# Kernel tuning notes

Measured on AMD Instinct MI355X. Metric: run time of the kernel, lower is better.

## Reference

```python
import jax, jax.numpy as jnp
import numpy as np

T = 4096          # tokens (batch*seq)
D = 768           # moe_intermediate_size (token hidden dim)
I = 2048          # intermediate_size (FFN inner dim)
E = 8             # num_experts


def setup_inputs() -> dict:
    key = jax.random.key(0)
    k_x, k_p, k_g, k_u, k_d = jax.random.split(key, 5)
    hidden_states = jax.random.normal(k_x, (T, D), dtype=jnp.float32)
    position_index = jax.random.randint(k_p, (T,), 0, E, dtype=jnp.int64)
    behavior_index = jnp.zeros((T,), dtype=jnp.int64)  # unused (behavior_injection=False)
    s = 0.02
    # torch Linear weight layout: [out_features, in_features]
    gate_w = jax.random.normal(k_g, (E, I, D), dtype=jnp.float32) * s
    up_w = jax.random.normal(k_u, (E, I, D), dtype=jnp.float32) * s
    down_w = jax.random.normal(k_d, (E, D, I), dtype=jnp.float32) * s
    return {
        "hidden_states": hidden_states,
        "position_index": position_index,
        "behavior_index": behavior_index,
        "gate_w": gate_w,
        "up_w": up_w,
        "down_w": down_w,
    }


def reference(hidden_states, position_index, behavior_index, gate_w, up_w, down_w):
    # Sparse MoE dispatch: each token routed to exactly one expert by position_index.
    # Dropout rate is 0.0 (eval) -> identity. behavior_injection=False -> behavior_index unused.
    num_experts = gate_w.shape[0]
    out = jnp.zeros_like(hidden_states)
    for e in range(num_experts):  # structural loop over fixed expert count
        mask = (position_index == e)[:, None]          # [T, 1]
        g = hidden_states @ gate_w[e].T                 # [T, I]
        u = hidden_states @ up_w[e].T                   # [T, I]
        y = (jax.nn.silu(g) * u) @ down_w[e].T          # [T, D]
        out = out + jnp.where(mask, y, 0.0)             # scatter-combine
    return out
```

## Files before the change

### kernel.cpp

```cpp
#include <hip/hip_runtime.h>
#include <hip/hip_bf16.h>

#define T_TOK 4096
#define DDIM  768
#define IDIM  2048
#define NEXP  8

typedef __attribute__((ext_vector_type(8))) short  bfrag;
typedef __attribute__((ext_vector_type(4))) float  ffrag;

static __device__ __forceinline__ unsigned short f2bf(float f) {
    union { float f; unsigned u; } v; v.f = f;
    unsigned r = v.u + 0x7FFFu + ((v.u >> 16) & 1u);
    return (unsigned short)(r >> 16);
}

static __device__ __forceinline__ unsigned cvt2(float x, float y) {
    return (unsigned)f2bf(x) | ((unsigned)f2bf(y) << 16);
}

__global__ void k_sort(const int* __restrict__ pos, int* __restrict__ ws_i,
                       int* __restrict__ perm) {
    __shared__ int hist[NEXP], cursor[NEXP];
    const int tid  = threadIdx.x;
    const int lane = tid & 63;
    if (tid < NEXP) hist[tid] = 0;
    __syncthreads();
    for (int i = tid; i < T_TOK; i += 1024) {
        int e = pos[i];
        #pragma unroll
        for (int ee = 0; ee < NEXP; ++ee) {
            unsigned long long m = __ballot(e == ee);
            if (e == ee && lane == (__ffsll((long long)m) - 1))
                atomicAdd(&hist[ee], __popcll(m));
        }
    }
    __syncthreads();
    if (tid == 0) {
        int s = 0;
        for (int e = 0; e < NEXP; ++e) {
            cursor[e] = s;
            ws_i[e] = hist[e];
            ws_i[16 + e] = s;
            s += hist[e];
        }
        ws_i[16 + NEXP] = s;
    }
    __syncthreads();
    for (int i = tid; i < T_TOK; i += 1024) {
        int e = pos[i];
        int p = 0;
        #pragma unroll
        for (int ee = 0; ee < NEXP; ++ee) {
            unsigned long long m = __ballot(e == ee);
            if (e == ee) {
                int leader = __ffsll((long long)m) - 1;
                int rank = __popcll(m & ((1ull << lane) - 1ull));
                int base = 0;
                if (lane == leader) base = atomicAdd(&cursor[ee], __popcll(m));
                base = __shfl(base, leader);
                p = base + rank;
            }
        }
        perm[p] = i;
    }
}

__global__ void k_gather(const float* __restrict__ x, const int* __restrict__ perm,
                         unsigned short* __restrict__ xg) {
    int p = blockIdx.x;
    int tok = perm[p];
    int j = threadIdx.x * 4;
    const float4 v = *reinterpret_cast<const float4*>(x + (size_t)tok * DDIM + j);
    uint2 o;
    o.x = cvt2(v.x, v.y);
    o.y = cvt2(v.z, v.w);
    *reinterpret_cast<uint2*>(xg + (size_t)p * DDIM + j) = o;
}

__launch_bounds__(256, 2)
__global__ void k_gemm1(const unsigned short* __restrict__ xg,
                        const float* __restrict__ gate_w,
                        const float* __restrict__ up_w,
                        unsigned short* __restrict__ hg,
                        const int* __restrict__ ws_i) {
    const int e   = blockIdx.z;
    const int cnt = ws_i[e];
    if (cnt == 0) return;
    const int nmt = (cnt + 127) >> 7;
    const int mg  = blockIdx.y;
    if (mg >= nmt) return;
    const int off = ws_i[16 + e];
    const int n0  = blockIdx.x * 64;

    const int tid  = threadIdx.x;
    const int lane = tid & 63;
    const int wave = tid >> 6;
    const int wm   = wave & 1;
    const int wn   = wave >> 1;

    __shared__ __align__(16) unsigned short lsA[128 * 56];
    __shared__ __align__(16) unsigned short lsG[64 * 56];
    __shared__ __align__(16) unsigned short lsU[64 * 56];

    const float* gate_e = gate_w + (size_t)e * (IDIM * DDIM);
    const float* up_e   = up_w   + (size_t)e * (IDIM * DDIM);

    const int ar = tid >> 2;
    const int aq = tid & 3;
    const int br = tid >> 3;
    const int bq = tid & 7;

    const float* gp0 = gate_e + (size_t)(n0 + br)      * DDIM + bq * 4;
    const float* gp1 = gate_e + (size_t)(n0 + br + 32) * DDIM + bq * 4;
    const float* up0 = up_e   + (size_t)(n0 + br)      * DDIM + bq * 4;
    const float* up1 = up_e   + (size_t)(n0 + br + 32) * DDIM + bq * 4;

    const int koff = (lane >> 4) * 8;
    const int rsel = lane & 15;
    const int colb  = lane & 15;
    const int rquad = (lane >> 4) * 4;

    for (int mt = mg; mt < nmt; mt += 2) {
        const int m0 = mt * 128;
        int g0 = off + m0 + ar;      if (g0 > T_TOK - 1) g0 = T_TOK - 1;
        int g1 = off + m0 + ar + 64; if (g1 > T_TOK - 1) g1 = T_TOK - 1;
        const unsigned short* a0p = xg + (size_t)g0 * DDIM + aq * 8;
        const unsigned short* a1p = xg + (size_t)g1 * DDIM + aq * 8;

        uint4  pa0 = *reinterpret_cast<const uint4*>(a0p);
        uint4  pa1 = *reinterpret_cast<const uint4*>(a1p);
        float4 pg0 = *reinterpret_cast<const float4*>(gp0);
        float4 pg1 = *reinterpret_cast<const float4*>(gp1);
        float4 pu0 = *reinterpret_cast<const float4*>(up0);
        float4 pu1 = *reinterpret_cast<const float4*>(up1);

        ffrag accG[4][2], accU[4][2];
        const ffrag fz = {0.f, 0.f, 0.f, 0.f};
        #pragma unroll
        for (int mi = 0; mi < 4; ++mi)
            #pragma unroll
            for (int ni = 0; ni < 2; ++ni) { accG[mi][ni] = fz; accU[mi][ni] = fz; }

        for (int kt = 0; kt < DDIM / 32; ++kt) {
            *reinterpret_cast<uint4*>(&lsA[ar * 56 + aq * 8])        = pa0;
            *reinterpret_cast<uint4*>(&lsA[(ar + 64) * 56 + aq * 8]) = pa1;
            { uint2 o; o.x = cvt2(pg0.x, pg0.y); o.y = cvt2(pg0.z, pg0.w);
              *reinterpret_cast<uint2*>(&lsG[br * 56 + bq * 4]) = o; }
            { uint2 o; o.x = cvt2(pg1.x, pg1.y); o.y = cvt2(pg1.z, pg1.w);
              *reinterpret_cast<uint2*>(&lsG[(br + 32) * 56 + bq * 4]) = o; }
            { uint2 o; o.x = cvt2(pu0.x, pu0.y); o.y = cvt2(pu0.z, pu0.w);
              *reinterpret_cast<uint2*>(&lsU[br * 56 + bq * 4]) = o; }
            { uint2 o; o.x = cvt2(pu1.x, pu1.y); o.y = cvt2(pu1.z, pu1.w);
              *reinterpret_cast<uint2*>(&lsU[(br + 32) * 56 + bq * 4]) = o; }
            __syncthreads();

            if (kt < DDIM / 32 - 1) {
                const int kb = (kt + 1) * 32;
                pa0 = *reinterpret_cast<const uint4*>(a0p + kb);
                pa1 = *reinterpret_cast<const uint4*>(a1p + kb);
                pg0 = *reinterpret_cast<const float4*>(gp0 + kb);
                pg1 = *reinterpret_cast<const float4*>(gp1 + kb);
                pu0 = *reinterpret_cast<const float4*>(up0 + kb);
                pu1 = *reinterpret_cast<const float4*>(up1 + kb);
            }

            bfrag a[4], bg[2], bu[2];
            #pragma unroll
            for (int mi = 0; mi < 4; ++mi)
                a[mi] = *reinterpret_cast<const bfrag*>(&lsA[(wm * 64 + mi * 16 + rsel) * 56 + koff]);
            #pragma unroll
            for (int ni = 0; ni < 2; ++ni) {
                bg[ni] = *reinterpret_cast<const bfrag*>(&lsG[(wn * 32 + ni * 16 + rsel) * 56 + koff]);
                bu[ni] = *reinterpret_cast<const bfrag*>(&lsU[(wn * 32 + ni * 16 + rsel) * 56 + koff]);
            }
            #pragma unroll
            for (int mi = 0; mi < 4; ++mi)
                #pragma unroll
                for (int ni = 0; ni < 2; ++ni) {
                    accG[mi][ni] = __builtin_amdgcn_mfma_f32_16x16x32_bf16(a[mi], bg[ni], accG[mi][ni], 0, 0, 0);
                    accU[mi][ni] = __builtin_amdgcn_mfma_f32_16x16x32_bf16(a[mi], bu[ni], accU[mi][ni], 0, 0, 0);
                }
            __syncthreads();
        }

        #pragma unroll
        for (int mi = 0; mi < 4; ++mi)
            #pragma unroll
            for (int ni = 0; ni < 2; ++ni) {
                int n = n0 + wn * 32 + ni * 16 + colb;
                #pragma unroll
                for (int r = 0; r < 4; ++r) {
                    int ml = wm * 64 + mi * 16 + rquad + r;
                    if (m0 + ml < cnt) {
                        float g = accG[mi][ni][r];
                        float u = accU[mi][ni][r];
                        float h = (g / (1.0f + __expf(-g))) * u;
                        hg[(size_t)(off + m0 + ml) * IDIM + n] = f2bf(h);
                    }
                }
            }
    }
}

__launch_bounds__(256, 2)
__global__ void k_gemm2(const unsigned short* __restrict__ hg,
                        const float* __restrict__ down_w,
                        float* __restrict__ out,
                        const int* __restrict__ ws_i,
                        const int* __restrict__ perm) {
    const int e   = blockIdx.y;
    const int cnt = ws_i[e];
    if (cnt == 0) return;
    const int nmt = (cnt + 127) >> 7;
    const int mg  = blockIdx.z;
    if (mg >= nmt) return;
    const int off = ws_i[16 + e];
    const int n0  = blockIdx.x * 64;

    const int tid  = threadIdx.x;
    const int lane = tid & 63;
    const int wave = tid >> 6;
    const int wm   = wave & 1;
    const int wn   = wave >> 1;

    __shared__ __align__(16) unsigned short lsA[128 * 56];
    __shared__ __align__(16) unsigned short lsB[64 * 56];

    const float* down_e = down_w + (size_t)e * (DDIM * IDIM);

    const int ar = tid >> 2;
    const int aq = tid & 3;
    const int br = tid >> 3;
    const int bq = tid & 7;

    const float* bp0 = down_e + (size_t)(n0 + br)      * IDIM + bq * 4;
    const float* bp1 = down_e + (size_t)(n0 + br + 32) * IDIM + bq * 4;

    const int koff = (lane >> 4) * 8;
    const int rsel = lane & 15;
    const int colb  = lane & 15;
    const int rquad = (lane >> 4) * 4;

    for (int mt = mg; mt < nmt; mt += 4) {
        const int m0 = mt * 128;
        int g0 = off + m0 + ar;      if (g0 > T_TOK - 1) g0 = T_TOK - 1;
        int g1 = off + m0 + ar + 64; if (g1 > T_TOK - 1) g1 = T_TOK - 1;
        const unsigned short* a0p = hg + (size_t)g0 * IDIM + aq * 8;
        const unsigned short* a1p = hg + (size_t)g1 * IDIM + aq * 8;

        uint4  pa0 = *reinterpret_cast<const uint4*>(a0p);
        uint4  pa1 = *reinterpret_cast<const uint4*>(a1p);
        float4 pb0 = *reinterpret_cast<const float4*>(bp0);
        float4 pb1 = *reinterpret_cast<const float4*>(bp1);

        ffrag acc[4][2];
        const ffrag fz = {0.f, 0.f, 0.f, 0.f};
        #pragma unroll
        for (int mi = 0; mi < 4; ++mi)
            #pragma unroll
            for (int ni = 0; ni < 2; ++ni) acc[mi][ni] = fz;

        for (int kt = 0; kt < IDIM / 32; ++kt) {
            *reinterpret_cast<uint4*>(&lsA[ar * 56 + aq * 8])        = pa0;
            *reinterpret_cast<uint4*>(&lsA[(ar + 64) * 56 + aq * 8]) = pa1;
            { uint2 o; o.x = cvt2(pb0.x, pb0.y); o.y = cvt2(pb0.z, pb0.w);
              *reinterpret_cast<uint2*>(&lsB[br * 56 + bq * 4]) = o; }
            { uint2 o; o.x = cvt2(pb1.x, pb1.y); o.y = cvt2(pb1.z, pb1.w);
              *reinterpret_cast<uint2*>(&lsB[(br + 32) * 56 + bq * 4]) = o; }
            __syncthreads();

            if (kt < IDIM / 32 - 1) {
                const int kb = (kt + 1) * 32;
                pa0 = *reinterpret_cast<const uint4*>(a0p + kb);
                pa1 = *reinterpret_cast<const uint4*>(a1p + kb);
                pb0 = *reinterpret_cast<const float4*>(bp0 + kb);
                pb1 = *reinterpret_cast<const float4*>(bp1 + kb);
            }

            bfrag a[4], b[2];
            #pragma unroll
            for (int mi = 0; mi < 4; ++mi)
                a[mi] = *reinterpret_cast<const bfrag*>(&lsA[(wm * 64 + mi * 16 + rsel) * 56 + koff]);
            #pragma unroll
            for (int ni = 0; ni < 2; ++ni)
                b[ni] = *reinterpret_cast<const bfrag*>(&lsB[(wn * 32 + ni * 16 + rsel) * 56 + koff]);
            #pragma unroll
            for (int mi = 0; mi < 4; ++mi)
                #pragma unroll
                for (int ni = 0; ni < 2; ++ni)
                    acc[mi][ni] = __builtin_amdgcn_mfma_f32_16x16x32_bf16(a[mi], b[ni], acc[mi][ni], 0, 0, 0);
            __syncthreads();
        }

        #pragma unroll
        for (int mi = 0; mi < 4; ++mi)
            #pragma unroll
            for (int r = 0; r < 4; ++r) {
                int ml = wm * 64 + mi * 16 + rquad + r;
                if (m0 + ml < cnt) {
                    int tok = perm[off + m0 + ml];
                    float* orow = out + (size_t)tok * DDIM + n0 + wn * 32 + colb;
                    orow[0]  = acc[mi][0][r];
                    orow[16] = acc[mi][1][r];
                }
            }
    }
}

extern "C" void kernel_launch(void* const* d_in, const int* in_sizes, int n_in,
                              void* d_out, int out_size, void* d_ws, size_t ws_size,
                              hipStream_t stream) {
    const float* x      = (const float*)d_in[0];
    const int*   pos    = (const int*)d_in[1];
    const float* gate_w = (const float*)d_in[3];
    const float* up_w   = (const float*)d_in[4];
    const float* down_w = (const float*)d_in[5];
    float* out = (float*)d_out;

    char* ws = (char*)d_ws;
    int* ws_i = (int*)ws;
    int* perm = (int*)(ws + 1024);
    unsigned short* xg = (unsigned short*)(ws + 32768);
    unsigned short* hg = (unsigned short*)(ws + (8u << 20));

    k_sort<<<dim3(1), dim3(1024), 0, stream>>>(pos, ws_i, perm);
    k_gather<<<dim3(T_TOK), dim3(192), 0, stream>>>(x, perm, xg);

    dim3 g1(IDIM / 64, 2, NEXP);
    k_gemm1<<<g1, dim3(256), 0, stream>>>(xg, gate_w, up_w, hg, ws_i);
    dim3 g2(DDIM / 64, NEXP, 4);
    k_gemm2<<<g2, dim3(256), 0, stream>>>(hg, down_w, out, ws_i, perm);
}
```

Baseline: 346.4 us.

## Pre-convert weights to bf16 and rebuild expert GEMMs with direct LDS loads and split-K

Measured after the change: 327.3 us. 1.06x faster.

```diff
diff --git a/kernel.cpp b/kernel.cpp
--- a/kernel.cpp
+++ b/kernel.cpp
@@ -18,6 +18,10 @@
 static __device__ __forceinline__ unsigned cvt2(float x, float y) {
     return (unsigned)f2bf(x) | ((unsigned)f2bf(y) << 16);
 }
+
+#define GL2LDS(gp, lp) __builtin_amdgcn_global_load_lds(                      \
+    (const __attribute__((address_space(1))) void*)(const void*)(gp),          \
+    (__attribute__((address_space(3))) void*)(lp), 16, 0, 0)
 
 __global__ void k_sort(const int* __restrict__ pos, int* __restrict__ ws_i,
                        int* __restrict__ perm) {
@@ -78,20 +82,142 @@
     *reinterpret_cast<uint2*>(xg + (size_t)p * DDIM + j) = o;
 }
 
+__global__ void k_wconv(const float* __restrict__ g, const float* __restrict__ u,
+                        const float* __restrict__ d,
+                        unsigned short* __restrict__ wg,
+                        unsigned short* __restrict__ wu,
+                        unsigned short* __restrict__ wd) {
+    const int C = NEXP * IDIM * DDIM / 4;
+    for (int i = blockIdx.x * blockDim.x + threadIdx.x; i < 3 * C;
+         i += gridDim.x * blockDim.x) {
+        const float* src; unsigned short* dst; int off;
+        if (i < C)          { src = g; dst = wg; off = i; }
+        else if (i < 2 * C) { src = u; dst = wu; off = i - C; }
+        else                { src = d; dst = wd; off = i - 2 * C; }
+        float4 v = reinterpret_cast<const float4*>(src)[off];
+        uint2 o;
+        o.x = cvt2(v.x, v.y);
+        o.y = cvt2(v.z, v.w);
+        reinterpret_cast<uint2*>(dst)[off] = o;
+    }
+}
+
 __launch_bounds__(256, 2)
 __global__ void k_gemm1(const unsigned short* __restrict__ xg,
-                        const float* __restrict__ gate_w,
-                        const float* __restrict__ up_w,
+                        const unsigned short* __restrict__ wg,
+                        const unsigned short* __restrict__ wu,
                         unsigned short* __restrict__ hg,
                         const int* __restrict__ ws_i) {
     const int e   = blockIdx.z;
     const int cnt = ws_i[e];
-    if (cnt == 0) return;
-    const int nmt = (cnt + 127) >> 7;
-    const int mg  = blockIdx.y;
-    if (mg >= nmt) return;
+    const int m0  = blockIdx.y * 128;
+    if (cnt == 0 || m0 >= cnt) return;
     const int off = ws_i[16 + e];
-    const int n0  = blockIdx.x * 64;
+    const int nt  = blockIdx.x;
+
+    __shared__ __align__(16) unsigned char smem[32768];
+    unsigned short* lsA = (unsigned short*)smem;
+    unsigned short* lsB = (unsigned short*)(smem + 8192);
+    float*          lsX = (float*)smem;
+
+    const int tid  = threadIdx.x;
+    const int lane = tid & 63;
+    const int wave = tid >> 6;
+    const int wm   = wave & 1;
+    const int wsel = wave >> 1;
+
+    const int arow = tid >> 2;
+    const int aq   = tid & 3;
+
+    const unsigned short* gA0 = xg + (size_t)(off + m0 + arow) * DDIM + aq * 8;
+    const unsigned short* gA1 = gA0 + (size_t)64 * DDIM;
+    const unsigned short* gB0 = wg + ((size_t)e * IDIM + nt * 64 + arow) * DDIM + aq * 8;
+    const unsigned short* gB1 = wu + ((size_t)e * IDIM + nt * 64 + arow) * DDIM + aq * 8;
+    unsigned short* lA0 = lsA + tid * 8;
+    unsigned short* lA1 = lsA + 2048 + tid * 8;
+    unsigned short* lB0 = lsB + tid * 8;
+    unsigned short* lB1 = lsB + 2048 + tid * 8;
+
+    ffrag acc[4][4];
+    const ffrag fz = {0.f, 0.f, 0.f, 0.f};
+    #pragma unroll
+    for (int mi = 0; mi < 4; ++mi)
+        #pragma unroll
+        for (int ni = 0; ni < 4; ++ni) acc[mi][ni] = fz;
+
+    const int koff = (lane >> 4) * 8;
+    const int rsel = lane & 15;
+
+    for (int kt = 0; kt < DDIM / 32; ++kt) {
+        const int kb = kt * 32;
+        GL2LDS(gA0 + kb, lA0);
+        GL2LDS(gA1 + kb, lA1);
+        GL2LDS(gB0 + kb, lB0);
+        GL2LDS(gB1 + kb, lB1);
+        __syncthreads();
+
+        bfrag a[4], b[4];
+        #pragma unroll
+        for (int mi = 0; mi < 4; ++mi)
+            a[mi] = *reinterpret_cast<const bfrag*>(&lsA[(wm * 64 + mi * 16 + rsel) * 32 + koff]);
+        #pragma unroll
+        for (int ni = 0; ni < 4; ++ni)
+            b[ni] = *reinterpret_cast<const bfrag*>(&lsB[(wsel * 64 + ni * 16 + rsel) * 32 + koff]);
+        #pragma unroll
+        for (int mi = 0; mi < 4; ++mi)
+            #pragma unroll
+            for (int ni = 0; ni < 4; ++ni)
+                acc[mi][ni] = __builtin_amdgcn_mfma_f32_16x16x32_bf16(a[mi], b[ni], acc[mi][ni], 0, 0, 0);
+        __syncthreads();
+    }
+
+    const int colb  = lane & 15;
+    const int rquad = (lane >> 4) * 4;
+    if (wsel == 1) {
+        #pragma unroll
+        for (int mi = 0; mi < 4; ++mi)
+            #pragma unroll
+            for (int ni = 0; ni < 4; ++ni)
+                #pragma unroll
+                for (int r = 0; r < 4; ++r)
+                    lsX[(wm * 64 + mi * 16 + rquad + r) * 64 + ni * 16 + colb] = acc[mi][ni][r];
+    }
+    __syncthreads();
+    if (wsel == 0) {
+        #pragma unroll
+        for (int mi = 0; mi < 4; ++mi)
+            #pragma unroll
+            for (int ni = 0; ni < 4; ++ni)
+                #pragma unroll
+                for (int r = 0; r < 4; ++r) {
+                    int ml = wm * 64 + mi * 16 + rquad + r;
+                    if (m0 + ml < cnt) {
+                        float gv = acc[mi][ni][r];
+                        float uv = lsX[ml * 64 + ni * 16 + colb];
+                        float h  = (gv / (1.0f + __expf(-gv))) * uv;
+                        hg[(size_t)(off + m0 + ml) * IDIM + nt * 64 + ni * 16 + colb] = f2bf(h);
+                    }
+                }
+    }
+}
+
+__launch_bounds__(256, 2)
+__global__ void k_gemm2(const unsigned short* __restrict__ hg,
+                        const unsigned short* __restrict__ wd,
+                        float* __restrict__ out,
+                        const int* __restrict__ ws_i,
+                        const int* __restrict__ perm) {
+    const int e   = blockIdx.z & 7;
+    const int s   = blockIdx.z >> 3;
+    const int cnt = ws_i[e];
+    const int m0  = blockIdx.y * 128;
+    if (cnt == 0 || m0 >= cnt) return;
+    const int off = ws_i[16 + e];
+    const int n0  = blockIdx.x * 128;
+
+    __shared__ __align__(16) unsigned char smem[16384];
+    unsigned short* lsA = (unsigned short*)smem;
+    unsigned short* lsB = (unsigned short*)(smem + 8192);
 
     const int tid  = threadIdx.x;
     const int lane = tid & 63;
@@ -99,213 +225,66 @@
     const int wm   = wave & 1;
     const int wn   = wave >> 1;
 
-    __shared__ __align__(16) unsigned short lsA[128 * 56];
-    __shared__ __align__(16) unsigned short lsG[64 * 56];
-    __shared__ __align__(16) unsigned short lsU[64 * 56];
-
-    const float* gate_e = gate_w + (size_t)e * (IDIM * DDIM);
-    const float* up_e   = up_w   + (size_t)e * (IDIM * DDIM);
-
-    const int ar = tid >> 2;
-    const int aq = tid & 3;
-    const int br = tid >> 3;
-    const int bq = tid & 7;
-
-    const float* gp0 = gate_e + (size_t)(n0 + br)      * DDIM + bq * 4;
-    const float* gp1 = gate_e + (size_t)(n0 + br + 32) * DDIM + bq * 4;
-    const float* up0 = up_e   + (size_t)(n0 + br)      * DDIM + bq * 4;
-    const float* up1 = up_e   + (size_t)(n0 + br + 32) * DDIM + bq * 4;
+    const int arow = tid >> 2;
+    const int aq   = tid & 3;
+
+    const unsigned short* gA0 = hg + (size_t)(off + m0 + arow) * IDIM + s * 512 + aq * 8;
+    const unsigned short* gA1 = gA0 + (size_t)64 * IDIM;
+    const unsigned short* gB0 = wd + ((size_t)e * DDIM + n0 + arow) * IDIM + s * 512 + aq * 8;
+    const unsigned short* gB1 = gB0 + (size_t)64 * IDIM;
+    unsigned short* lA0 = lsA + tid * 8;
+    unsigned short* lA1 = lsA + 2048 + tid * 8;
+    unsigned short* lB0 = lsB + tid * 8;
+    unsigned short* lB1 = lsB + 2048 + tid * 8;
+
+    ffrag acc[4][4];
+    const ffrag fz = {0.f, 0.f, 0.f, 0.f};
+    #pragma unroll
+    for (int mi = 0; mi < 4; ++mi)
+        #pragma unroll
+        for (int ni = 0; ni < 4; ++ni) acc[mi][ni] = fz;
 
     const int koff = (lane >> 4) * 8;
     const int rsel = lane & 15;
+
+    for (int kt = 0; kt < 16; ++kt) {
+        const int kb = kt * 32;
+        GL2LDS(gA0 + kb, lA0);
+        GL2LDS(gA1 + kb, lA1);
+        GL2LDS(gB0 + kb, lB0);
+        GL2LDS(gB1 + kb, lB1);
+        __syncthreads();
+
+        bfrag a[4], b[4];
+        #pragma unroll
+        for (int mi = 0; mi < 4; ++mi)
+            a[mi] = *reinterpret_cast<const bfrag*>(&lsA[(wm * 64 + mi * 16 + rsel) * 32 + koff]);
+        #pragma unroll
+        for (int ni = 0; ni < 4; ++ni)
+            b[ni] = *reinterpret_cast<const bfrag*>(&lsB[(wn * 64 + ni * 16 + rsel) * 32 + koff]);
+        #pragma unroll
+        for (int mi = 0; mi < 4; ++mi)
+            #pragma unroll
+            for (int ni = 0; ni < 4; ++ni)
+                acc[mi][ni] = __builtin_amdgcn_mfma_f32_16x16x32_bf16(a[mi], b[ni], acc[mi][ni], 0, 0, 0);
+        __syncthreads();
+    }
+
     const int colb  = lane & 15;
     const int rquad = (lane >> 4) * 4;
-
-    for (int mt = mg; mt < nmt; mt += 2) {
-        const int m0 = mt * 128;
-        int g0 = off + m0 + ar;      if (g0 > T_TOK - 1) g0 = T_TOK - 1;
-        int g1 = off + m0 + ar + 64; if (g1 > T_TOK - 1) g1 = T_TOK - 1;
-        const unsigned short* a0p = xg + (size_t)g0 * DDIM + aq * 8;
-        const unsigned short* a1p = xg + (size_t)g1 * DDIM + aq * 8;
-
-        uint4  pa0 = *reinterpret_cast<const uint4*>(a0p);
-        uint4  pa1 = *reinterpret_cast<const uint4*>(a1p);
-        float4 pg0 = *reinterpret_cast<const float4*>(gp0);
-        float4 pg1 = *reinterpret_cast<const float4*>(gp1);
-        float4 pu0 = *reinterpret_cast<const float4*>(up0);
-        float4 pu1 = *reinterpret_cast<const float4*>(up1);
-
-        ffrag accG[4][2], accU[4][2];
-        const ffrag fz = {0.f, 0.f, 0.f, 0.f};
-        #pragma unroll
-        for (int mi = 0; mi < 4; ++mi)
-            #pragma unroll
-            for (int ni = 0; ni < 2; ++ni) { accG[mi][ni] = fz; accU[mi][ni] = fz; }
-
-        for (int kt = 0; kt < DDIM / 32; ++kt) {
-            *reinterpret_cast<uint4*>(&lsA[ar * 56 + aq * 8])        = pa0;
-            *reinterpret_cast<uint4*>(&lsA[(ar + 64) * 56 + aq * 8]) = pa1;
-            { uint2 o; o.x = cvt2(pg0.x, pg0.y); o.y = cvt2(pg0.z, pg0.w);
-              *reinterpret_cast<uint2*>(&lsG[br * 56 + bq * 4]) = o; }
-            { uint2 o; o.x = cvt2(pg1.x, pg1.y); o.y = cvt2(pg1.z, pg1.w);
-              *reinterpret_cast<uint2*>(&lsG[(br + 32) * 56 + bq * 4]) = o; }
-            { uint2 o; o.x = cvt2(pu0.x, pu0.y); o.y = cvt2(pu0.z, pu0.w);
-              *reinterpret_cast<uint2*>(&lsU[br * 56 + bq * 4]) = o; }
-            { uint2 o; o.x = cvt2(pu1.x, pu1.y); o.y = cvt2(pu1.z, pu1.w);
-              *reinterpret_cast<uint2*>(&lsU[(br + 32) * 56 + bq * 4]) = o; }
-            __syncthreads();
-
-            if (kt < DDIM / 32 - 1) {
-                const int kb = (kt + 1) * 32;
-                pa0 = *reinterpret_cast<const uint4*>(a0p + kb);
-                pa1 = *reinterpret_cast<const uint4*>(a1p + kb);
-                pg0 = *reinterpret_cast<const float4*>(gp0 + kb);
-                pg1 = *reinterpret_cast<const float4*>(gp1 + kb);
-                pu0 = *reinterpret_cast<const float4*>(up0 + kb);
-                pu1 = *reinterpret_cast<const float4*>(up1 + kb);
+    #pragma unroll
+    for (int mi = 0; mi < 4; ++mi)
+        #pragma unroll
+        for (int r = 0; r < 4; ++r) {
+            int ml = wm * 64 + mi * 16 + rquad + r;
+            if (m0 + ml < cnt) {
+                int tok = perm[off + m0 + ml];
+                float* orow = out + (size_t)tok * DDIM + n0 + wn * 64 + colb;
+                #pragma unroll
+                for (int ni = 0; ni < 4; ++ni)
+                    unsafeAtomicAdd(orow + ni * 16, acc[mi][ni][r]);
             }
-
-            bfrag a[4], bg[2], bu[2];
-            #pragma unroll
-            for (int mi = 0; mi < 4; ++mi)
-                a[mi] = *reinterpret_cast<const bfrag*>(&lsA[(wm * 64 + mi * 16 + rsel) * 56 + koff]);
-            #pragma unroll
-            for (int ni = 0; ni < 2; ++ni) {
-                bg[ni] = *reinterpret_cast<const bfrag*>(&lsG[(wn * 32 + ni * 16 + rsel) * 56 + koff]);
-                bu[ni] = *reinterpret_cast<const bfrag*>(&lsU[(wn * 32 + ni * 16 + rsel) * 56 + koff]);
-            }
-            #pragma unroll
-            for (int mi = 0; mi < 4; ++mi)
-                #pragma unroll
-                for (int ni = 0; ni < 2; ++ni) {
-                    accG[mi][ni] = __builtin_amdgcn_mfma_f32_16x16x32_bf16(a[mi], bg[ni], accG[mi][ni], 0, 0, 0);
-                    accU[mi][ni] = __builtin_amdgcn_mfma_f32_16x16x32_bf16(a[mi], bu[ni], accU[mi][ni], 0, 0, 0);
-                }
-            __syncthreads();
         }
-
-        #pragma unroll
-        for (int mi = 0; mi < 4; ++mi)
-            #pragma unroll
-            for (int ni = 0; ni < 2; ++ni) {
-                int n = n0 + wn * 32 + ni * 16 + colb;
-                #pragma unroll
-                for (int r = 0; r < 4; ++r) {
-                    int ml = wm * 64 + mi * 16 + rquad + r;
-                    if (m0 + ml < cnt) {
-                        float g = accG[mi][ni][r];
-                        float u = accU[mi][ni][r];
-                        float h = (g / (1.0f + __expf(-g))) * u;
-                        hg[(size_t)(off + m0 + ml) * IDIM + n] = f2bf(h);
-                    }
-                }
-            }
-    }
-}
-
-__launch_bounds__(256, 2)
-__global__ void k_gemm2(const unsigned short* __restrict__ hg,
-                        const float* __restrict__ down_w,
-                        float* __restrict__ out,
-                        const int* __restrict__ ws_i,
-                        const int* __restrict__ perm) {
-    const int e   = blockIdx.y;
-    const int cnt = ws_i[e];
-    if (cnt == 0) return;
-    const int nmt = (cnt + 127) >> 7;
-    const int mg  = blockIdx.z;
-    if (mg >= nmt) return;
-    const int off = ws_i[16 + e];
-    const int n0  = blockIdx.x * 64;
-
-    const int tid  = threadIdx.x;
-    const int lane = tid & 63;
-    const int wave = tid >> 6;
-    const int wm   = wave & 1;
-    const int wn   = wave >> 1;
-
-    __shared__ __align__(16) unsigned short lsA[128 * 56];
-    __shared__ __align__(16) unsigned short lsB[64 * 56];
-
-    const float* down_e = down_w + (size_t)e * (DDIM * IDIM);
-
-    const int ar = tid >> 2;
-    const int aq = tid & 3;
-    const int br = tid >> 3;
-    const int bq = tid & 7;
-
-    const float* bp0 = down_e + (size_t)(n0 + br)      * IDIM + bq * 4;
-    const float* bp1 = down_e + (size_t)(n0 + br + 32) * IDIM + bq * 4;
-
-    const int koff = (lane >> 4) * 8;
-    const int rsel = lane & 15;
-    const int colb  = lane & 15;
-    const int rquad = (lane >> 4) * 4;
-
-    for (int mt = mg; mt < nmt; mt += 4) {
-        const int m0 = mt * 128;
-        int g0 = off + m0 + ar;      if (g0 > T_TOK - 1) g0 = T_TOK - 1;
-        int g1 = off + m0 + ar + 64; if (g1 > T_TOK - 1) g1 = T_TOK - 1;
-        const unsigned short* a0p = hg + (size_t)g0 * IDIM + aq * 8;
-        const unsigned short* a1p = hg + (size_t)g1 * IDIM + aq * 8;
-
-        uint4  pa0 = *reinterpret_cast<const uint4*>(a0p);
-        uint4  pa1 = *reinterpret_cast<const uint4*>(a1p);
-        float4 pb0 = *reinterpret_cast<const float4*>(bp0);
-        float4 pb1 = *reinterpret_cast<const float4*>(bp1);
-
-        ffrag acc[4][2];
-        const ffrag fz = {0.f, 0.f, 0.f, 0.f};
-        #pragma unroll
-        for (int mi = 0; mi < 4; ++mi)
-            #pragma unroll
-            for (int ni = 0; ni < 2; ++ni) acc[mi][ni] = fz;
-
-        for (int kt = 0; kt < IDIM / 32; ++kt) {
-            *reinterpret_cast<uint4*>(&lsA[ar * 56 + aq * 8])        = pa0;
-            *reinterpret_cast<uint4*>(&lsA[(ar + 64) * 56 + aq * 8]) = pa1;
-            { uint2 o; o.x = cvt2(pb0.x, pb0.y); o.y = cvt2(pb0.z, pb0.w);
-              *reinterpret_cast<uint2*>(&lsB[br * 56 + bq * 4]) = o; }
-            { uint2 o; o.x = cvt2(pb1.x, pb1.y); o.y = cvt2(pb1.z, pb1.w);
-              *reinterpret_cast<uint2*>(&lsB[(br + 32) * 56 + bq * 4]) = o; }
-            __syncthreads();
-
-            if (kt < IDIM / 32 - 1) {
-                const int kb = (kt + 1) * 32;
-                pa0 = *reinterpret_cast<const uint4*>(a0p + kb);
-                pa1 = *reinterpret_cast<const uint4*>(a1p + kb);
-                pb0 = *reinterpret_cast<const float4*>(bp0 + kb);
-                pb1 = *reinterpret_cast<const float4*>(bp1 + kb);
-            }
-
-            bfrag a[4], b[2];
-            #pragma unroll
-            for (int mi = 0; mi < 4; ++mi)
-                a[mi] = *reinterpret_cast<const bfrag*>(&lsA[(wm * 64 + mi * 16 + rsel) * 56 + koff]);
-            #pragma unroll
-            for (int ni = 0; ni < 2; ++ni)
-                b[ni] = *reinterpret_cast<const bfrag*>(&lsB[(wn * 32 + ni * 16 + rsel) * 56 + koff]);
-            #pragma unroll
-            for (int mi = 0; mi < 4; ++mi)
-                #pragma unroll
-                for (int ni = 0; ni < 2; ++ni)
-                    acc[mi][ni] = __builtin_amdgcn_mfma_f32_16x16x32_bf16(a[mi], b[ni], acc[mi][ni], 0, 0, 0);
-            __syncthreads();
-        }
-
-        #pragma unroll
-        for (int mi = 0; mi < 4; ++mi)
-            #pragma unroll
-            for (int r = 0; r < 4; ++r) {
-                int ml = wm * 64 + mi * 16 + rquad + r;
-                if (m0 + ml < cnt) {
-                    int tok = perm[off + m0 + ml];
-                    float* orow = out + (size_t)tok * DDIM + n0 + wn * 32 + colb;
-                    orow[0]  = acc[mi][0][r];
-                    orow[16] = acc[mi][1][r];
-                }
-            }
-    }
 }
 
 extern "C" void kernel_launch(void* const* d_in, const int* in_sizes, int n_in,
@@ -322,13 +301,18 @@
     int* ws_i = (int*)ws;
     int* perm = (int*)(ws + 1024);
     unsigned short* xg = (unsigned short*)(ws + 32768);
-    unsigned short* hg = (unsigned short*)(ws + (8u << 20));
-
+    unsigned short* hg = (unsigned short*)(ws + (8ull  << 20));
+    unsigned short* wg = (unsigned short*)(ws + (26ull << 20));
+    unsigned short* wu = (unsigned short*)(ws + (52ull << 20));
+    unsigned short* wd = (unsigned short*)(ws + (78ull << 20));
+
+    (void)hipMemsetAsync(d_out, 0, (size_t)out_size * sizeof(float), stream);
     k_sort<<<dim3(1), dim3(1024), 0, stream>>>(pos, ws_i, perm);
     k_gather<<<dim3(T_TOK), dim3(192), 0, stream>>>(x, perm, xg);
-
-    dim3 g1(IDIM / 64, 2, NEXP);
-    k_gemm1<<<g1, dim3(256), 0, stream>>>(xg, gate_w, up_w, hg, ws_i);
-    dim3 g2(DDIM / 64, NEXP, 4);
-    k_gemm2<<<g2, dim3(256), 0, stream>>>(hg, down_w, out, ws_i, perm);
-}
+    k_wconv<<<dim3(3072), dim3(256), 0, stream>>>(gate_w, up_w, down_w, wg, wu, wd);
+
+    dim3 g1(IDIM / 64, 32, NEXP);
+    k_gemm1<<<g1, dim3(256), 0, stream>>>(xg, wg, wu, hg, ws_i);
+    dim3 g2(DDIM / 128, 32, NEXP * 4);
+    k_gemm2<<<g2, dim3(256), 0, stream>>>(hg, wd, out, ws_i, perm);
+}
```
